# Kernel tuning notes

Hardware: AMD Instinct MI355X
Metric: run time of the kernel (lower is better)

## Reference

```python
import jax, jax.numpy as jnp
import numpy as np

NUM_EMB = 1024
EMB_DIM = 32


def setup_inputs() -> dict:
    key = jax.random.key(0)
    k1, k2 = jax.random.split(key)
    z = jax.random.normal(k1, (32, EMB_DIM, 64, 64), dtype=jnp.float32)
    # nn.Embedding weight init: uniform(-1/num_embeddings, 1/num_embeddings)
    emb_weight = jax.random.uniform(
        k2, (NUM_EMB, EMB_DIM), dtype=jnp.float32,
        minval=-1.0 / NUM_EMB, maxval=1.0 / NUM_EMB)
    return {"z": z, "emb_weight": emb_weight}


def reference(z, emb_weight):
    # z: [B, C, H, W] -> [B, H, W, C]
    z_p = jnp.transpose(z, (0, 2, 3, 1))
    B, H, W, C = z_p.shape
    z_flat = z_p.reshape(-1, C)  # [N, C]
    # squared distances via expansion: ||z||^2 + ||e||^2 - 2 z.e  -> [N, K]
    d = (jnp.sum(z_flat * z_flat, axis=1, keepdims=True)
         + jnp.sum(emb_weight * emb_weight, axis=1)
         - 2.0 * jnp.matmul(z_flat, emb_weight.T))
    idx = jnp.argmin(d, axis=1)  # [N]
    z_q = emb_weight[idx].reshape(B, H, W, C)
    # straight-through estimator (applied in BHWC, then back to BCHW)
    z_q = z_p + jax.lax.stop_gradient(z_q - z_p)
    z_q = jnp.transpose(z_q, (0, 3, 1, 2))  # [B, C, H, W]
    return z_q, idx
```

## Files before the change

### kernel.cpp

```cpp
#include <hip/hip_runtime.h>


#define NUM_EMB 1024
#define EMB_DIM 32
#define HW      4096
#define BATCH   32
#define N_TOT   (BATCH * HW)
#define NSPLIT  4
#define CODES_PER (NUM_EMB / NSPLIT)
#define MARGIN  1.0e-4f
#define CHUNK   256
#define ESTRIDE 36
#define OVF_CAP 131072

#define OFF_BQ   0u
#define OFF_EH   4096u
#define OFF_EL   69632u
#define OFF_CNT  135168u
#define OFF_CAND 659456u
#define OFF_OVFC 4853760u
#define OFF_OVFL 4853776u
#define WS_NEED  5378064u
#define WS_NEED_R7 (4096u + 4u * 131072u * 8u)

using bf16x8 = __attribute__((ext_vector_type(8))) short;
using bf16x4 = __attribute__((ext_vector_type(4))) short;
using f32x4  = __attribute__((ext_vector_type(4))) float;

#define REPEAT32(M) \
    M(0)  M(1)  M(2)  M(3)  M(4)  M(5)  M(6)  M(7)  \
    M(8)  M(9)  M(10) M(11) M(12) M(13) M(14) M(15) \
    M(16) M(17) M(18) M(19) M(20) M(21) M(22) M(23) \
    M(24) M(25) M(26) M(27) M(28) M(29) M(30) M(31)

__device__ __forceinline__ unsigned short bf16_rne(float x) {
    unsigned u = __float_as_uint(x);
    return (unsigned short)((u + 0x7FFFu + ((u >> 16) & 1u)) >> 16);
}

__device__ __forceinline__ float pairwise_sq32(const float* __restrict__ e) {
    float r0 = __fmul_rn(e[0], e[0]), r1 = __fmul_rn(e[1], e[1]);
    float r2 = __fmul_rn(e[2], e[2]), r3 = __fmul_rn(e[3], e[3]);
    float r4 = __fmul_rn(e[4], e[4]), r5 = __fmul_rn(e[5], e[5]);
    float r6 = __fmul_rn(e[6], e[6]), r7 = __fmul_rn(e[7], e[7]);
#pragma unroll
    for (int i = 8; i < 32; i += 8) {
        r0 = __fadd_rn(r0, __fmul_rn(e[i + 0], e[i + 0]));
        r1 = __fadd_rn(r1, __fmul_rn(e[i + 1], e[i + 1]));
        r2 = __fadd_rn(r2, __fmul_rn(e[i + 2], e[i + 2]));
        r3 = __fadd_rn(r3, __fmul_rn(e[i + 3], e[i + 3]));
        r4 = __fadd_rn(r4, __fmul_rn(e[i + 4], e[i + 4]));
        r5 = __fadd_rn(r5, __fmul_rn(e[i + 5], e[i + 5]));
        r6 = __fadd_rn(r6, __fmul_rn(e[i + 6], e[i + 6]));
        r7 = __fadd_rn(r7, __fmul_rn(e[i + 7], e[i + 7]));
    }
    return __fadd_rn(__fadd_rn(__fadd_rn(r0, r1), __fadd_rn(r2, r3)),
                     __fadd_rn(__fadd_rn(r4, r5), __fadd_rn(r6, r7)));
}

__device__ __forceinline__ void store_row16(unsigned short* dst,
                                            const unsigned short* v) {
    unsigned w[16];
#pragma unroll
    for (int i = 0; i < 16; ++i)
        w[i] = (unsigned)v[2 * i] | ((unsigned)v[2 * i + 1] << 16);
    uint4* d4 = (uint4*)dst;
    d4[0] = make_uint4(w[0], w[1], w[2], w[3]);
    d4[1] = make_uint4(w[4], w[5], w[6], w[7]);
    d4[2] = make_uint4(w[8], w[9], w[10], w[11]);
    d4[3] = make_uint4(w[12], w[13], w[14], w[15]);
}

__global__ __launch_bounds__(256) void vq_prep_e(
        const float* __restrict__ emb, float* __restrict__ bq,
        unsigned short* __restrict__ eh, unsigned short* __restrict__ el,
        int* __restrict__ cnt, int* __restrict__ ovfc) {
    const int g = blockIdx.x * 256 + threadIdx.x;
    cnt[g] = 0;
    if (g == 0) *ovfc = 0;
    if (g >= NUM_EMB) return;
    const float* e = emb + g * EMB_DIM;
    bq[g] = pairwise_sq32(e);
    unsigned short h[32], l[32];
#pragma unroll
    for (int c = 0; c < 32; ++c) {
        float v = -2.0f * e[c];
        unsigned short hb = bf16_rne(v);
        float hf = __uint_as_float((unsigned)hb << 16);
        l[c] = bf16_rne(v - hf);
        h[c] = hb;
    }
    store_row16(eh + (size_t)g * 32, h);
    store_row16(el + (size_t)g * 32, l);
}

__device__ __forceinline__ bf16x8 lds_read8(const short* p) {
    bf16x4 a = *(const bf16x4*)p;
    bf16x4 b = *(const bf16x4*)(p + 4);
    return __builtin_shufflevector(a, b, 0, 1, 2, 3, 4, 5, 6, 7);
}

__global__ __launch_bounds__(256, 4) void vq_filter(
        const float* __restrict__ z,
        const unsigned short* __restrict__ eh,
        const unsigned short* __restrict__ el,
        const float* __restrict__ bq, int* __restrict__ cnt,
        int* __restrict__ cand) {
    __shared__ __align__(16) short seh[CHUNK * ESTRIDE];
    __shared__ __align__(16) short sel[CHUNK * ESTRIDE];
    __shared__ float sbq[CHUNK];

    const int tid  = threadIdx.x;
    const int lane = tid & 63;
    const int wv   = tid >> 6;
    const int cloc = lane & 15, quad = lane >> 4;
    const int qbase = blockIdx.x * 128 + wv * 32;

    bf16x8 azh[2], azl[2];
#pragma unroll
    for (int t = 0; t < 2; ++t) {
        const int q  = qbase + t * 16 + cloc;
        const int b  = q >> 12;
        const int hw = q & 4095;
        const float* zb = z + ((size_t)b * EMB_DIM + quad * 8) * HW + hw;
#pragma unroll
        for (int k = 0; k < 8; ++k) {
            float v = zb[(size_t)k * HW];
            unsigned short hb = bf16_rne(v);
            float hf = __uint_as_float((unsigned)hb << 16);
            azh[t][k] = (short)hb;
            azl[t][k] = (short)bf16_rne(v - hf);
        }
    }

    float m1[2][4], m2[2][4];
    int   i1[2][4];
#pragma unroll
    for (int t = 0; t < 2; ++t)
#pragma unroll
        for (int r = 0; r < 4; ++r) {
            m1[t][r] = 3.4e38f; m2[t][r] = 3.4e38f; i1[t][r] = 0;
        }

    for (int ch = 0; ch < 4; ++ch) {
        if (ch) __syncthreads();
#pragma unroll
        for (int i = 0; i < 8; ++i) {
            const int chunk = i * 256 + tid;
            const int r = chunk >> 3, c = chunk & 7;
            *(uint2*)&seh[r * ESTRIDE + c * 4] =
                *(const uint2*)(eh + (size_t)(ch * CHUNK + r) * 32 + c * 4);
            *(uint2*)&sel[r * ESTRIDE + c * 4] =
                *(const uint2*)(el + (size_t)(ch * CHUNK + r) * 32 + c * 4);
        }
        sbq[tid] = bq[ch * CHUNK + tid];
        __syncthreads();

        for (int jt = 0; jt < 16; ++jt) {
            const int row = jt * 16 + cloc;
            bf16x8 efh = lds_read8(&seh[row * ESTRIDE + quad * 8]);
            bf16x8 efl = lds_read8(&sel[row * ESTRIDE + quad * 8]);
            const float bqv = sbq[row];
            const int jts = ch * 16 + jt;
#pragma unroll
            for (int t = 0; t < 2; ++t) {
                f32x4 acc = {bqv, bqv, bqv, bqv};
                acc = __builtin_amdgcn_mfma_f32_16x16x32_bf16(azl[t], efh, acc, 0, 0, 0);
                acc = __builtin_amdgcn_mfma_f32_16x16x32_bf16(azh[t], efl, acc, 0, 0, 0);
                acc = __builtin_amdgcn_mfma_f32_16x16x32_bf16(azh[t], efh, acc, 0, 0, 0);
#pragma unroll
                for (int r = 0; r < 4; ++r) {
                    const float tt = acc[r];
                    const bool l1 = tt < m1[t][r];
                    const bool l2 = tt < m2[t][r];
                    m2[t][r] = l1 ? m1[t][r] : (l2 ? tt : m2[t][r]);
                    m1[t][r] = l1 ? tt  : m1[t][r];
                    i1[t][r] = l1 ? jts : i1[t][r];
                }
            }
        }
    }

    float g[2][4];
#pragma unroll
    for (int t = 0; t < 2; ++t)
#pragma unroll
        for (int r = 0; r < 4; ++r) g[t][r] = m1[t][r];
#pragma unroll
    for (int off = 1; off < 16; off <<= 1)
#pragma unroll
        for (int t = 0; t < 2; ++t)
#pragma unroll
            for (int r = 0; r < 4; ++r)
                g[t][r] = fminf(g[t][r], __shfl_xor(g[t][r], off, 64));

#pragma unroll
    for (int t = 0; t < 2; ++t)
#pragma unroll
        for (int r = 0; r < 4; ++r) {
            const float thr = g[t][r] + MARGIN;
            const int q = qbase + t * 16 + quad * 4 + r;
            if (m1[t][r] <= thr) {
                int pos = atomicAdd(&cnt[q], 1);
                if (pos < 8) cand[(q << 3) + pos] = i1[t][r] * 16 + cloc;
            }
            if (m2[t][r] <= thr) atomicAdd(&cnt[q], 1000);
        }
}

#define LOADZ(c) float z##c = zp[(size_t)(c) * HW];
#define Z_SQ_A()                                                              \
    float r0 = __fmul_rn(z0, z0), r1 = __fmul_rn(z1, z1);                     \
    float r2 = __fmul_rn(z2, z2), r3 = __fmul_rn(z3, z3);                     \
    float r4 = __fmul_rn(z4, z4), r5 = __fmul_rn(z5, z5);                     \
    float r6 = __fmul_rn(z6, z6), r7 = __fmul_rn(z7, z7);                     \
    r0 = __fadd_rn(r0, __fmul_rn(z8,  z8));  r0 = __fadd_rn(r0, __fmul_rn(z16, z16)); \
    r0 = __fadd_rn(r0, __fmul_rn(z24, z24));                                  \
    r1 = __fadd_rn(r1, __fmul_rn(z9,  z9));  r1 = __fadd_rn(r1, __fmul_rn(z17, z17)); \
    r1 = __fadd_rn(r1, __fmul_rn(z25, z25));                                  \
    r2 = __fadd_rn(r2, __fmul_rn(z10, z10)); r2 = __fadd_rn(r2, __fmul_rn(z18, z18)); \
    r2 = __fadd_rn(r2, __fmul_rn(z26, z26));                                  \
    r3 = __fadd_rn(r3, __fmul_rn(z11, z11)); r3 = __fadd_rn(r3, __fmul_rn(z19, z19)); \
    r3 = __fadd_rn(r3, __fmul_rn(z27, z27));                                  \
    r4 = __fadd_rn(r4, __fmul_rn(z12, z12)); r4 = __fadd_rn(r4, __fmul_rn(z20, z20)); \
    r4 = __fadd_rn(r4, __fmul_rn(z28, z28));                                  \
    r5 = __fadd_rn(r5, __fmul_rn(z13, z13)); r5 = __fadd_rn(r5, __fmul_rn(z21, z21)); \
    r5 = __fadd_rn(r5, __fmul_rn(z29, z29));                                  \
    r6 = __fadd_rn(r6, __fmul_rn(z14, z14)); r6 = __fadd_rn(r6, __fmul_rn(z22, z22)); \
    r6 = __fadd_rn(r6, __fmul_rn(z30, z30));                                  \
    r7 = __fadd_rn(r7, __fmul_rn(z15, z15)); r7 = __fadd_rn(r7, __fmul_rn(z23, z23)); \
    r7 = __fadd_rn(r7, __fmul_rn(z31, z31));                                  \
    const float a = __fadd_rn(                                                \
        __fadd_rn(__fadd_rn(r0, r1), __fadd_rn(r2, r3)),                      \
        __fadd_rn(__fadd_rn(r4, r5), __fadd_rn(r6, r7)));

#define FMA1(k) m = __fmaf_rn(z##k, e[(k)], m);
#define EXACT_KEY(jv)                                                         \
    {                                                                         \
        const float* e = emb + (size_t)(jv) * EMB_DIM;                        \
        float m = 0.0f;                                                       \
        REPEAT32(FMA1)                                                        \
        float d = __fsub_rn(__fadd_rn(a, bq[(jv)]), __fmul_rn(2.0f, m));      \
        unsigned u = __float_as_uint(d);                                      \
        u = (u & 0x80000000u) ? ~u : (u | 0x80000000u);                       \
        unsigned long long kk =                                               \
            ((unsigned long long)u << 32) | (unsigned)(jv);                   \
        if (kk < bestk) bestk = kk;                                           \
    }

__global__ __launch_bounds__(256, 2) void vq_pass3(
        const float* __restrict__ z, const float* __restrict__ emb,
        const float* __restrict__ bq, const int* __restrict__ cnt,
        const int* __restrict__ cand, int* __restrict__ ovfc,
        int* __restrict__ ovfl, float* __restrict__ out_zq,
        float* __restrict__ out_idx) {
    const int n  = blockIdx.x * 256 + threadIdx.x;
    const int b  = n >> 12;
    const int hw = n & 4095;
    const int c = cnt[n];
    if (c < 1 || c > 8) {
        int pos = atomicAdd(ovfc, 1);
        ovfl[pos] = n;
        return;
    }
    int bidx;
    if (c == 1) {
        bidx = cand[n << 3];
    } else {
        const float* zp = z + (size_t)b * EMB_DIM * HW + hw;
        REPEAT32(LOADZ)
        Z_SQ_A()
        unsigned long long bestk = ~0ull;
        for (int i = 0; i < c; ++i) { const int jv = cand[(n << 3) + i]; EXACT_KEY(jv) }
        bidx = (int)(unsigned)(bestk & 0xffffffffu);
    }
    out_idx[n] = (float)bidx;
    const float* eb = emb + (size_t)bidx * EMB_DIM;
    float* op = out_zq + (size_t)b * EMB_DIM * HW + hw;
#pragma unroll
    for (int cc = 0; cc < EMB_DIM; ++cc) op[(size_t)cc * HW] = eb[cc];
}

__global__ __launch_bounds__(256) void vq_fixup(
        const float* __restrict__ z, const float* __restrict__ emb,
        const float* __restrict__ bq, const int* __restrict__ ovfc,
        const int* __restrict__ ovfl, float* __restrict__ out_zq,
        float* __restrict__ out_idx) {
    __shared__ unsigned long long bs[256];
    const int tid = threadIdx.x;
    int total = *ovfc;
    if (total > OVF_CAP) total = OVF_CAP;

    for (int it = blockIdx.x; it < total; it += gridDim.x) {
        const int n  = ovfl[it];
        const int b  = n >> 12;
        const int hw = n & 4095;
        const float* zp = z + (size_t)b * EMB_DIM * HW + hw;
        REPEAT32(LOADZ)
        Z_SQ_A()
        unsigned long long bestk = ~0ull;
#pragma unroll
        for (int k = 0; k < 4; ++k) { const int jv = tid * 4 + k; EXACT_KEY(jv) }
        bs[tid] = bestk;
        __syncthreads();
        for (int off = 128; off > 0; off >>= 1) {
            if (tid < off && bs[tid + off] < bs[tid]) bs[tid] = bs[tid + off];
            __syncthreads();
        }
        const int bidx = (int)(unsigned)(bs[0] & 0xffffffffu);
        if (tid == 0) out_idx[n] = (float)bidx;
        if (tid < EMB_DIM)
            out_zq[(size_t)b * EMB_DIM * HW + (size_t)tid * HW + hw] =
                emb[(size_t)bidx * EMB_DIM + tid];
        __syncthreads();
    }
}

#define SCAN_GROUP4(j)                                                        \
    {                                                                         \
        const float* e = emb + (size_t)(j) * EMB_DIM;                         \
        const float bq0 = bq[(j) + 0], bq1 = bq[(j) + 1];                     \
        const float bq2 = bq[(j) + 2], bq3 = bq[(j) + 3];                     \
        float m0 = 0.0f, m1 = 0.0f, m2 = 0.0f, m3 = 0.0f;                     \
        REPEAT32(FMA_K)                                                       \
        float d0 = __fsub_rn(__fadd_rn(a, bq0), __fmul_rn(2.0f, m0));         \
        float d1 = __fsub_rn(__fadd_rn(a, bq1), __fmul_rn(2.0f, m1));         \
        float d2 = __fsub_rn(__fadd_rn(a, bq2), __fmul_rn(2.0f, m2));         \
        float d3 = __fsub_rn(__fadd_rn(a, bq3), __fmul_rn(2.0f, m3));         \
        if (d0 < best) { best = d0; bidx = (j) + 0; }                         \
        if (d1 < best) { best = d1; bidx = (j) + 1; }                         \
        if (d2 < best) { best = d2; bidx = (j) + 2; }                         \
        if (d3 < best) { best = d3; bidx = (j) + 3; }                         \
    }
#define FMA_K(k) \
        m0 = __fmaf_rn(z##k, e[0 * EMB_DIM + (k)], m0); \
        m1 = __fmaf_rn(z##k, e[1 * EMB_DIM + (k)], m1); \
        m2 = __fmaf_rn(z##k, e[2 * EMB_DIM + (k)], m2); \
        m3 = __fmaf_rn(z##k, e[3 * EMB_DIM + (k)], m3);

__global__ __launch_bounds__(256) void vq_sqnorm_kernel(
        const float* __restrict__ emb, float* __restrict__ bq) {
    int j = blockIdx.x * 256 + threadIdx.x;
    if (j < NUM_EMB) bq[j] = pairwise_sq32(emb + j * EMB_DIM);
}

__global__ __launch_bounds__(128, 4) void vq_partial_kernel(
        const float* __restrict__ z, const float* __restrict__ emb,
        const float* __restrict__ bq, unsigned long long* __restrict__ pk) {
    const int n  = blockIdx.x * 128 + threadIdx.x;
    const int b  = n >> 12;
    const int hw = n & 4095;
    const float* zp = z + (size_t)b * EMB_DIM * HW + hw;
    REPEAT32(LOADZ)
    Z_SQ_A()
    const int j0 = blockIdx.y * CODES_PER;
    float best = 3.4e38f;
    int   bidx = j0;
    for (int j = j0; j < j0 + CODES_PER; j += 4) SCAN_GROUP4(j)
    pk[(size_t)blockIdx.y * N_TOT + n] =
        ((unsigned long long)__float_as_uint(best) << 32) | (unsigned)bidx;
}

__global__ __launch_bounds__(256, 2) void vq_main_kernel(
        const float* __restrict__ z, const float* __restrict__ emb,
        const float* __restrict__ bq, float* __restrict__ out_zq,
        float* __restrict__ out_idx) {
    const int n  = blockIdx.x * 256 + threadIdx.x;
    const int b  = n >> 12;
    const int hw = n & 4095;
    const float* zp = z + (size_t)b * EMB_DIM * HW + hw;
    REPEAT32(LOADZ)
    Z_SQ_A()
    float best = 3.4e38f;
    int   bidx = 0;
    for (int j = 0; j < NUM_EMB; j += 4) SCAN_GROUP4(j)
    out_idx[n] = (float)bidx;
    const float* eb = emb + (size_t)bidx * EMB_DIM;
    float* op = out_zq + (size_t)b * EMB_DIM * HW + hw;
#pragma unroll
    for (int cc = 0; cc < EMB_DIM; ++cc) op[(size_t)cc * HW] = eb[cc];
}

__global__ __launch_bounds__(256) void vq_combine_kernel(
        const float* __restrict__ emb,
        const unsigned long long* __restrict__ pk,
        float* __restrict__ out_zq, float* __restrict__ out_idx) {
    const int n = blockIdx.x * 256 + threadIdx.x;
    unsigned long long m = pk[n];
#pragma unroll
    for (int y = 1; y < NSPLIT; ++y) {
        unsigned long long v = pk[(size_t)y * N_TOT + n];
        if (v < m) m = v;
    }
    const int bidx = (int)(unsigned)(m & 0xffffffffu);
    out_idx[n] = (float)bidx;
    const int b  = n >> 12;
    const int hw = n & 4095;
    const float* eb = emb + (size_t)bidx * EMB_DIM;
    float* op = out_zq + (size_t)b * EMB_DIM * HW + hw;
#pragma unroll
    for (int cc = 0; cc < EMB_DIM; ++cc) op[(size_t)cc * HW] = eb[cc];
}

extern "C" void kernel_launch(void* const* d_in, const int* in_sizes, int n_in,
                              void* d_out, int out_size, void* d_ws,
                              size_t ws_size, hipStream_t stream) {
    const float* z   = (const float*)d_in[0];
    const float* emb = (const float*)d_in[1];
    char* ws = (char*)d_ws;
    float* out0 = (float*)d_out;
    float* out1 = out0 + (size_t)BATCH * EMB_DIM * HW;

    if (ws_size >= WS_NEED) {
        float*          bq   = (float*)(ws + OFF_BQ);
        unsigned short* eh   = (unsigned short*)(ws + OFF_EH);
        unsigned short* el   = (unsigned short*)(ws + OFF_EL);
        int*            cnt  = (int*)(ws + OFF_CNT);
        int*            cand = (int*)(ws + OFF_CAND);
        int*            ovfc = (int*)(ws + OFF_OVFC);
        int*            ovfl = (int*)(ws + OFF_OVFL);

        vq_prep_e<<<N_TOT / 256, 256, 0, stream>>>(emb, bq, eh, el, cnt, ovfc);
        vq_filter<<<N_TOT / 128, 256, 0, stream>>>(z, eh, el, bq, cnt, cand);
        vq_pass3<<<N_TOT / 256, 256, 0, stream>>>(z, emb, bq, cnt, cand,
                                                  ovfc, ovfl, out0, out1);
        vq_fixup<<<1024, 256, 0, stream>>>(z, emb, bq, ovfc, ovfl,
                                           out0, out1);
    } else if (ws_size >= WS_NEED_R7) {
        float* bq = (float*)ws;
        unsigned long long* pk = (unsigned long long*)(ws + 4096);
        vq_sqnorm_kernel<<<NUM_EMB / 256, 256, 0, stream>>>(emb, bq);
        vq_partial_kernel<<<dim3(N_TOT / 128, NSPLIT), 128, 0, stream>>>(
            z, emb, bq, pk);
        vq_combine_kernel<<<N_TOT / 256, 256, 0, stream>>>(emb, pk, out0, out1);
    } else {
        float* bq = (float*)ws;
        vq_sqnorm_kernel<<<NUM_EMB / 256, 256, 0, stream>>>(emb, bq);
        vq_main_kernel<<<N_TOT / 256, 256, 0, stream>>>(z, emb, bq, out0, out1);
    }
}
```

Before: 140.5 us.

## Resolve unique candidates in filter, compact rescore lists, add separate writeback

The filter kernel now uses wave ballots to classify each query. A single candidate writes its index directly. Two to four candidates are appended to a compact rescore list, and ambiguous or second-best cases go to a fixup list. The old per-query pass3 is replaced by a grid-stride rescore over only the listed queries, and z_q output moves into a separate writeback kernel. The top-2 tracking also switches to fmed3/fmin. This removes most per-query exact rescoring and scattered atomics, at the cost of an extra launch and a re-read of indices.

```diff
diff --git a/kernel.cpp b/kernel.cpp
--- a/kernel.cpp
+++ b/kernel.cpp
@@ -11,16 +11,16 @@
 #define MARGIN  1.0e-4f
 #define CHUNK   256
 #define ESTRIDE 36
-#define OVF_CAP 131072
-
-#define OFF_BQ   0u
-#define OFF_EH   4096u
-#define OFF_EL   69632u
-#define OFF_CNT  135168u
-#define OFF_CAND 659456u
-#define OFF_OVFC 4853760u
-#define OFF_OVFL 4853776u
-#define WS_NEED  5378064u
+
+#define OFF_BQ    0u
+#define OFF_EH    4096u
+#define OFF_EL    69632u
+#define OFF_CNT   135168u
+#define OFF_CAND  659456u
+#define OFF_CTRS  2756608u
+#define OFF_LISTA 2756624u
+#define OFF_LISTB 3280912u
+#define WS_NEED   3805200u
 #define WS_NEED_R7 (4096u + 4u * 131072u * 8u)
 
 using bf16x8 = __attribute__((ext_vector_type(8))) short;
@@ -74,10 +74,10 @@
 __global__ __launch_bounds__(256) void vq_prep_e(
         const float* __restrict__ emb, float* __restrict__ bq,
         unsigned short* __restrict__ eh, unsigned short* __restrict__ el,
-        int* __restrict__ cnt, int* __restrict__ ovfc) {
+        int* __restrict__ cnt, int* __restrict__ ctrs) {
     const int g = blockIdx.x * 256 + threadIdx.x;
     cnt[g] = 0;
-    if (g == 0) *ovfc = 0;
+    if (g < 2) ctrs[g] = 0;
     if (g >= NUM_EMB) return;
     const float* e = emb + g * EMB_DIM;
     bq[g] = pairwise_sq32(e);
@@ -105,7 +105,9 @@
         const unsigned short* __restrict__ eh,
         const unsigned short* __restrict__ el,
         const float* __restrict__ bq, int* __restrict__ cnt,
-        int* __restrict__ cand) {
+        int* __restrict__ cand, int* __restrict__ ctrs,
+        int* __restrict__ listA, int* __restrict__ listB,
+        float* __restrict__ out_idx) {
     __shared__ __align__(16) short seh[CHUNK * ESTRIDE];
     __shared__ __align__(16) short sel[CHUNK * ESTRIDE];
     __shared__ float sbq[CHUNK];
@@ -172,9 +174,8 @@
                 for (int r = 0; r < 4; ++r) {
                     const float tt = acc[r];
                     const bool l1 = tt < m1[t][r];
-                    const bool l2 = tt < m2[t][r];
-                    m2[t][r] = l1 ? m1[t][r] : (l2 ? tt : m2[t][r]);
-                    m1[t][r] = l1 ? tt  : m1[t][r];
+                    m2[t][r] = __builtin_amdgcn_fmed3f(tt, m1[t][r], m2[t][r]);
+                    m1[t][r] = fminf(m1[t][r], tt);
                     i1[t][r] = l1 ? jts : i1[t][r];
                 }
             }
@@ -199,12 +200,26 @@
 #pragma unroll
         for (int r = 0; r < 4; ++r) {
             const float thr = g[t][r] + MARGIN;
-            const int q = qbase + t * 16 + quad * 4 + r;
-            if (m1[t][r] <= thr) {
-                int pos = atomicAdd(&cnt[q], 1);
-                if (pos < 8) cand[(q << 3) + pos] = i1[t][r] * 16 + cloc;
+            const int   q   = qbase + t * 16 + quad * 4 + r;
+            const bool  f1  = m1[t][r] <= thr;
+            const bool  f2  = m2[t][r] <= thr;
+            const unsigned long long b1 = __ballot(f1);
+            const unsigned long long b2 = __ballot(f2);
+            const unsigned mk1 = (unsigned)(b1 >> (quad * 16)) & 0xFFFFu;
+            const unsigned mk2 = (unsigned)(b2 >> (quad * 16)) & 0xFFFFu;
+            const int pc  = __popc(mk1);
+            const int ldr = __ffs(mk1) - 1;
+            if (mk2 | (unsigned)(pc > 4)) {
+                if (cloc == ldr) { int p = atomicAdd(&ctrs[1], 1); listB[p] = q; }
+            } else if (pc == 1) {
+                if (f1) out_idx[q] = (float)(i1[t][r] * 16 + cloc);
+            } else {
+                if (f1) {
+                    int pos = atomicAdd(&cnt[q], 1);
+                    cand[(q << 2) + pos] = i1[t][r] * 16 + cloc;
+                }
+                if (cloc == ldr) { int p = atomicAdd(&ctrs[0], 1); listA[p] = q; }
             }
-            if (m2[t][r] <= thr) atomicAdd(&cnt[q], 1000);
         }
 }
 
@@ -248,51 +263,37 @@
         if (kk < bestk) bestk = kk;                                           \
     }
 
-__global__ __launch_bounds__(256, 2) void vq_pass3(
+__global__ __launch_bounds__(256, 2) void vq_rescore(
         const float* __restrict__ z, const float* __restrict__ emb,
         const float* __restrict__ bq, const int* __restrict__ cnt,
-        const int* __restrict__ cand, int* __restrict__ ovfc,
-        int* __restrict__ ovfl, float* __restrict__ out_zq,
-        float* __restrict__ out_idx) {
-    const int n  = blockIdx.x * 256 + threadIdx.x;
-    const int b  = n >> 12;
-    const int hw = n & 4095;
-    const int c = cnt[n];
-    if (c < 1 || c > 8) {
-        int pos = atomicAdd(ovfc, 1);
-        ovfl[pos] = n;
-        return;
-    }
-    int bidx;
-    if (c == 1) {
-        bidx = cand[n << 3];
-    } else {
+        const int* __restrict__ cand, const int* __restrict__ ctrs,
+        const int* __restrict__ listA, float* __restrict__ out_idx) {
+    const int total = ctrs[0];
+    for (int i = blockIdx.x * 256 + threadIdx.x; i < total;
+         i += gridDim.x * 256) {
+        const int n  = listA[i];
+        const int b  = n >> 12;
+        const int hw = n & 4095;
         const float* zp = z + (size_t)b * EMB_DIM * HW + hw;
         REPEAT32(LOADZ)
         Z_SQ_A()
+        const int c = cnt[n];
         unsigned long long bestk = ~0ull;
-        for (int i = 0; i < c; ++i) { const int jv = cand[(n << 3) + i]; EXACT_KEY(jv) }
-        bidx = (int)(unsigned)(bestk & 0xffffffffu);
-    }
-    out_idx[n] = (float)bidx;
-    const float* eb = emb + (size_t)bidx * EMB_DIM;
-    float* op = out_zq + (size_t)b * EMB_DIM * HW + hw;
-#pragma unroll
-    for (int cc = 0; cc < EMB_DIM; ++cc) op[(size_t)cc * HW] = eb[cc];
+        for (int k = 0; k < c; ++k) { const int jv = cand[(n << 2) + k]; EXACT_KEY(jv) }
+        out_idx[n] = (float)(unsigned)(bestk & 0xffffffffu);
+    }
 }
 
 __global__ __launch_bounds__(256) void vq_fixup(
         const float* __restrict__ z, const float* __restrict__ emb,
-        const float* __restrict__ bq, const int* __restrict__ ovfc,
-        const int* __restrict__ ovfl, float* __restrict__ out_zq,
-        float* __restrict__ out_idx) {
+        const float* __restrict__ bq, const int* __restrict__ ctrs,
+        const int* __restrict__ listB, float* __restrict__ out_idx) {
     __shared__ unsigned long long bs[256];
     const int tid = threadIdx.x;
-    int total = *ovfc;
-    if (total > OVF_CAP) total = OVF_CAP;
+    const int total = ctrs[1];
 
     for (int it = blockIdx.x; it < total; it += gridDim.x) {
-        const int n  = ovfl[it];
+        const int n  = listB[it];
         const int b  = n >> 12;
         const int hw = n & 4095;
         const float* zp = z + (size_t)b * EMB_DIM * HW + hw;
@@ -307,12 +308,27 @@
             if (tid < off && bs[tid + off] < bs[tid]) bs[tid] = bs[tid + off];
             __syncthreads();
         }
-        const int bidx = (int)(unsigned)(bs[0] & 0xffffffffu);
-        if (tid == 0) out_idx[n] = (float)bidx;
-        if (tid < EMB_DIM)
-            out_zq[(size_t)b * EMB_DIM * HW + (size_t)tid * HW + hw] =
-                emb[(size_t)bidx * EMB_DIM + tid];
+        if (tid == 0) out_idx[n] = (float)(unsigned)(bs[0] & 0xffffffffu);
         __syncthreads();
+    }
+}
+
+__global__ __launch_bounds__(256) void vq_writeback(
+        const float* __restrict__ emb, const float* __restrict__ out_idx,
+        float* __restrict__ out_zq) {
+    const int n = blockIdx.x * 256 + threadIdx.x;
+    const int bidx = (int)out_idx[n];
+    const int b  = n >> 12;
+    const int hw = n & 4095;
+    const float4* er = (const float4*)(emb + (size_t)bidx * EMB_DIM);
+    float* op = out_zq + (size_t)b * EMB_DIM * HW + hw;
+#pragma unroll
+    for (int c4 = 0; c4 < 8; ++c4) {
+        float4 v = er[c4];
+        op[(size_t)(c4 * 4 + 0) * HW] = v.x;
+        op[(size_t)(c4 * 4 + 1) * HW] = v.y;
+        op[(size_t)(c4 * 4 + 2) * HW] = v.z;
+        op[(size_t)(c4 * 4 + 3) * HW] = v.w;
     }
 }
 
@@ -412,20 +428,22 @@
     float* out1 = out0 + (size_t)BATCH * EMB_DIM * HW;
 
     if (ws_size >= WS_NEED) {
-        float*          bq   = (float*)(ws + OFF_BQ);
-        unsigned short* eh   = (unsigned short*)(ws + OFF_EH);
-        unsigned short* el   = (unsigned short*)(ws + OFF_EL);
-        int*            cnt  = (int*)(ws + OFF_CNT);
-        int*            cand = (int*)(ws + OFF_CAND);
-        int*            ovfc = (int*)(ws + OFF_OVFC);
-        int*            ovfl = (int*)(ws + OFF_OVFL);
-
-        vq_prep_e<<<N_TOT / 256, 256, 0, stream>>>(emb, bq, eh, el, cnt, ovfc);
-        vq_filter<<<N_TOT / 128, 256, 0, stream>>>(z, eh, el, bq, cnt, cand);
-        vq_pass3<<<N_TOT / 256, 256, 0, stream>>>(z, emb, bq, cnt, cand,
-                                                  ovfc, ovfl, out0, out1);
-        vq_fixup<<<1024, 256, 0, stream>>>(z, emb, bq, ovfc, ovfl,
-                                           out0, out1);
+        float*          bq    = (float*)(ws + OFF_BQ);
+        unsigned short* eh    = (unsigned short*)(ws + OFF_EH);
+        unsigned short* el    = (unsigned short*)(ws + OFF_EL);
+        int*            cnt   = (int*)(ws + OFF_CNT);
+        int*            cand  = (int*)(ws + OFF_CAND);
+        int*            ctrs  = (int*)(ws + OFF_CTRS);
+        int*            listA = (int*)(ws + OFF_LISTA);
+        int*            listB = (int*)(ws + OFF_LISTB);
+
+        vq_prep_e<<<N_TOT / 256, 256, 0, stream>>>(emb, bq, eh, el, cnt, ctrs);
+        vq_filter<<<N_TOT / 128, 256, 0, stream>>>(z, eh, el, bq, cnt, cand,
+                                                   ctrs, listA, listB, out1);
+        vq_rescore<<<256, 256, 0, stream>>>(z, emb, bq, cnt, cand, ctrs,
+                                            listA, out1);
+        vq_fixup<<<1024, 256, 0, stream>>>(z, emb, bq, ctrs, listB, out1);
+        vq_writeback<<<N_TOT / 256, 256, 0, stream>>>(emb, out1, out0);
     } else if (ws_size >= WS_NEED_R7) {
         float* bq = (float*)ws;
         unsigned long long* pk = (unsigned long long*)(ws + 4096);
```

Result: slower. 216.7 us (+54.3%).
